# Kernel optimization log

Measured on AMD Instinct MI355X. Metric: run time of the kernel, lower is better.

The kernel has to match this reference:

```python
import jax, jax.numpy as jnp
import numpy as np

N_ENT = 2000
GAT_EMB = 64
GAT_HID = 3
HIDDEN = 256
BATCH = 8
ALPHA = 0.2  # LeakyReLU negative slope
MASK_FILL = jnp.float32(9e-15)  # original fills masked-out logits with 9e-15 (NOT -inf)


def setup_inputs() -> dict:
    key = jax.random.key(0)
    k1, k2, k3, k4, k5, k6 = jax.random.split(key, 6)
    emb = jax.random.normal(k1, (N_ENT, GAT_EMB), dtype=jnp.float32)
    W = jax.random.normal(k2, (GAT_EMB, GAT_HID), dtype=jnp.float32) * 0.2
    a = jax.random.normal(k3, (2 * GAT_HID, 1), dtype=jnp.float32) * 0.2
    fc1_w = jax.random.normal(k4, (HIDDEN, N_ENT * GAT_HID), dtype=jnp.float32) * 0.02
    fc1_b = jax.random.normal(k5, (HIDDEN,), dtype=jnp.float32) * 0.02
    adj = jax.random.randint(k6, (BATCH, N_ENT, N_ENT), 0, 2, dtype=jnp.int32)
    return {"emb": emb, "W": W, "a": a, "fc1_w": fc1_w, "fc1_b": fc1_b, "adj": adj}


def reference(emb, W, a, fc1_w, fc1_b, adj):
    # h = emb @ W : [N, 3] -- shared across all graphs in the batch
    h = emb @ W
    # Pairwise logits: original concatenates [h_i, h_j] and dots with a;
    # equivalent to (h @ a1)_i + (h @ a2)_j via broadcasting (no O(N^2*2H) tensor).
    s1 = h @ a[:GAT_HID, 0]   # [N]
    s2 = h @ a[GAT_HID:, 0]   # [N]
    e = jax.nn.leaky_relu(s1[:, None] + s2[None, :], negative_slope=ALPHA)  # [N, N]
    # Mask by adjacency (fill 9e-15, matching original), softmax over neighbors (dim=1)
    masked = jnp.where(adj > 0, e[None, :, :], MASK_FILL)  # [B, N, N]
    att = jax.nn.softmax(masked, axis=2)
    # Weighted aggregation + ELU (concat=True head)
    h_prime = jnp.einsum('bij,jd->bid', att, h)  # [B, N, 3]
    x = jax.nn.elu(h_prime).reshape(att.shape[0], -1)  # [B, N*3]
    return x @ fc1_w.T + fc1_b  # [B, hidden]
```

## Files before the change

### kernel.cpp

```cpp
#include <hip/hip_runtime.h>
#include <cstddef>

#define N_ENT   2000
#define GAT_EMB 64
#define HIDDEN  256
#define BATCH   8
#define ALPHA   0.2f

typedef _Float16 half4 __attribute__((ext_vector_type(4)));

#define WS_HX_OFF      8192
#define WS_HY_OFF      12288
#define WS_HZ_OFF      16384
#define WS_S1_OFF      20480
#define WS_X_OFF       28672
#define WS_TABLE_BYTES 28672
#define WS_TIER2_BYTES 124672

__global__ __launch_bounds__(256) void k_init(const float* __restrict__ fc1_b,
                                              float* __restrict__ out) {
    int idx = blockIdx.x * 256 + threadIdx.x;
    out[idx] = fc1_b[idx & (HIDDEN - 1)];
}

__global__ __launch_bounds__(256) void k_prep(const float* __restrict__ emb,
                                              const float* __restrict__ W,
                                              const float* __restrict__ a,
                                              float* __restrict__ ws) {
    __shared__ float sW[GAT_EMB * 3];
    __shared__ float sa[6];
    int t = threadIdx.x;
    if (t < GAT_EMB * 3) sW[t] = W[t];
    if (t < 6)           sa[t] = a[t];
    __syncthreads();
    int i = blockIdx.x * 256 + t;
    if (i >= 2048) return;
    if (i >= N_ENT) {
        ws[i] = 0.f;
        ((_Float16*)((char*)ws + WS_HX_OFF))[i] = (_Float16)0;
        ((_Float16*)((char*)ws + WS_HY_OFF))[i] = (_Float16)0;
        ((_Float16*)((char*)ws + WS_HZ_OFF))[i] = (_Float16)0;
        ws[WS_S1_OFF / 4 + i] = 0.f;
        return;
    }
    const float4* er = (const float4*)(emb + (size_t)i * GAT_EMB);
    float h0 = 0.f, h1 = 0.f, h2 = 0.f;
#pragma unroll
    for (int k4 = 0; k4 < GAT_EMB / 4; ++k4) {
        float4 e4 = er[k4];
        int k = 4 * k4;
        h0 += e4.x * sW[(k + 0) * 3 + 0]; h1 += e4.x * sW[(k + 0) * 3 + 1]; h2 += e4.x * sW[(k + 0) * 3 + 2];
        h0 += e4.y * sW[(k + 1) * 3 + 0]; h1 += e4.y * sW[(k + 1) * 3 + 1]; h2 += e4.y * sW[(k + 1) * 3 + 2];
        h0 += e4.z * sW[(k + 2) * 3 + 0]; h1 += e4.z * sW[(k + 2) * 3 + 1]; h2 += e4.z * sW[(k + 2) * 3 + 2];
        h0 += e4.w * sW[(k + 3) * 3 + 0]; h1 += e4.w * sW[(k + 3) * 3 + 1]; h2 += e4.w * sW[(k + 3) * 3 + 2];
    }
    ws[i] = h0 * sa[3] + h1 * sa[4] + h2 * sa[5];
    ((_Float16*)((char*)ws + WS_HX_OFF))[i] = (_Float16)h0;
    ((_Float16*)((char*)ws + WS_HY_OFF))[i] = (_Float16)h1;
    ((_Float16*)((char*)ws + WS_HZ_OFF))[i] = (_Float16)h2;
    ws[WS_S1_OFF / 4 + i] = h0 * sa[0] + h1 * sa[1] + h2 * sa[2];
}

__global__ __launch_bounds__(256, 4) void k_main(const float* __restrict__ emb,
                                                 const float* __restrict__ W,
                                                 const float* __restrict__ a,
                                                 const float* __restrict__ fc1_w,
                                                 const int*   __restrict__ adj,
                                                 float* __restrict__ wsf,
                                                 int mode,
                                                 float* __restrict__ out) {
    __shared__ __align__(16) unsigned char smem[20480];
    float*    s2s = (float*)smem;
    _Float16* hxs = (_Float16*)(smem + 8192);
    _Float16* hys = (_Float16*)(smem + 12288);
    _Float16* hzs = (_Float16*)(smem + 16384);
    __shared__ float sW[GAT_EMB * 3];
    __shared__ float sa[6];
    __shared__ float s1sh[16];
    __shared__ float xblk[48];

    int t = threadIdx.x;
    int R0 = blockIdx.x * 16;
    int b  = R0 / N_ENT;
    int i_base = R0 - b * N_ENT;

    if (mode != 0) {
        const uint4* src = (const uint4*)wsf;
        uint4* dst = (uint4*)smem;
#pragma unroll
        for (int rep = 0; rep < 5; ++rep) dst[rep * 256 + t] = src[rep * 256 + t];
        if (t < 16) s1sh[t] = wsf[WS_S1_OFF / 4 + i_base + t];
    } else {
        if (t < GAT_EMB * 3) sW[t] = W[t];
        if (t < 6)           sa[t] = a[t];
        __syncthreads();
        for (int j = t; j < N_ENT; j += 256) {
            const float4* er = (const float4*)(emb + (size_t)j * GAT_EMB);
            float h0 = 0.f, h1 = 0.f, h2 = 0.f;
#pragma unroll
            for (int k4 = 0; k4 < GAT_EMB / 4; ++k4) {
                float4 e4 = er[k4];
                int k = 4 * k4;
                h0 += e4.x * sW[(k + 0) * 3 + 0]; h1 += e4.x * sW[(k + 0) * 3 + 1]; h2 += e4.x * sW[(k + 0) * 3 + 2];
                h0 += e4.y * sW[(k + 1) * 3 + 0]; h1 += e4.y * sW[(k + 1) * 3 + 1]; h2 += e4.y * sW[(k + 1) * 3 + 2];
                h0 += e4.z * sW[(k + 2) * 3 + 0]; h1 += e4.z * sW[(k + 2) * 3 + 1]; h2 += e4.z * sW[(k + 2) * 3 + 2];
                h0 += e4.w * sW[(k + 3) * 3 + 0]; h1 += e4.w * sW[(k + 3) * 3 + 1]; h2 += e4.w * sW[(k + 3) * 3 + 2];
            }
            s2s[j] = h0 * sa[3] + h1 * sa[4] + h2 * sa[5];
            hxs[j] = (_Float16)h0; hys[j] = (_Float16)h1; hzs[j] = (_Float16)h2;
            if (j >= i_base && j < i_base + 16)
                s1sh[j - i_base] = h0 * sa[0] + h1 * sa[1] + h2 * sa[2];
        }
        if (t < 2048 - N_ENT) {
            int j = N_ENT + t;
            s2s[j] = 0.f; hxs[j] = (_Float16)0; hys[j] = (_Float16)0; hzs[j] = (_Float16)0;
        }
    }
    __syncthreads();

    int lane = t & 63;
    int w    = t >> 6;
    float s1r[4];
    const int* __restrict__ rowp[4];
#pragma unroll
    for (int r = 0; r < 4; ++r) {
        s1r[r] = s1sh[4 * w + r];
        rowp[r] = adj + ((size_t)b * N_ENT + (i_base + 4 * w + r)) * N_ENT;
    }

    float acc[4][4];
#pragma unroll
    for (int r = 0; r < 4; ++r) { acc[r][0] = 0.f; acc[r][1] = 0.f; acc[r][2] = 0.f; acc[r][3] = 0.f; }

    int l4 = lane << 2;
    int4 buf[3][4];
#pragma unroll
    for (int r = 0; r < 4; ++r) buf[0][r] = *(const int4*)(rowp[r] + l4);
#pragma unroll
    for (int r = 0; r < 4; ++r) buf[1][r] = *(const int4*)(rowp[r] + 256 + l4);

#pragma unroll
    for (int c = 0; c < 8; ++c) {
        if (c + 2 < 8) {
            int j2 = (c + 2) * 256 + l4;
            int jc2 = (j2 < N_ENT) ? j2 : 0;
#pragma unroll
            for (int r = 0; r < 4; ++r)
                buf[(c + 2) % 3][r] = *(const int4*)(rowp[r] + jc2);
        }
        int j0 = c * 256 + l4;
        bool valid = (j0 < N_ENT);
        float vw = valid ? 1.0f : 0.0f;
        float4 s2v = *(const float4*)&s2s[j0];
        half4  hxv = *(const half4*)&hxs[j0];
        half4  hyv = *(const half4*)&hys[j0];
        half4  hzv = *(const half4*)&hzs[j0];
        float hx[4], hy[4], hz[4];
#pragma unroll
        for (int q = 0; q < 4; ++q) { hx[q] = (float)hxv[q]; hy[q] = (float)hyv[q]; hz[q] = (float)hzv[q]; }
#pragma unroll
        for (int r = 0; r < 4; ++r) {
            const int* mi = (const int*)&buf[c % 3][r];
#pragma unroll
            for (int q = 0; q < 4; ++q) {
                float e  = s1r[r] + ((const float*)&s2v)[q];
                float ev = __expf(fmaxf(e, 0.f) + ALPHA * fminf(e, 0.f));
                float contrib = ((mi[q] > 0) ? ev : 1.0f) * vw;
                acc[r][0] += contrib;
                acc[r][1] += contrib * hx[q];
                acc[r][2] += contrib * hy[q];
                acc[r][3] += contrib * hz[q];
            }
        }
    }

#pragma unroll
    for (int off = 32; off > 0; off >>= 1)
#pragma unroll
        for (int r = 0; r < 4; ++r) {
            acc[r][0] += __shfl_xor(acc[r][0], off, 64);
            acc[r][1] += __shfl_xor(acc[r][1], off, 64);
            acc[r][2] += __shfl_xor(acc[r][2], off, 64);
            acc[r][3] += __shfl_xor(acc[r][3], off, 64);
        }

    if (lane == 0) {
#pragma unroll
        for (int r = 0; r < 4; ++r) {
            float inv = 1.f / acc[r][0];
            float p0 = acc[r][1] * inv, p1 = acc[r][2] * inv, p2 = acc[r][3] * inv;
            p0 = (p0 > 0.f) ? p0 : expm1f(p0);
            p1 = (p1 > 0.f) ? p1 : expm1f(p1);
            p2 = (p2 > 0.f) ? p2 : expm1f(p2);
            if (mode == 2) {
                _Float16* x16 = (_Float16*)((char*)wsf + WS_X_OFF);
                int i = i_base + 4 * w + r;
                x16[(size_t)(3 * i + 0) * 8 + b] = (_Float16)p0;
                x16[(size_t)(3 * i + 1) * 8 + b] = (_Float16)p1;
                x16[(size_t)(3 * i + 2) * 8 + b] = (_Float16)p2;
            } else {
                int cc = 3 * (4 * w + r);
                xblk[cc + 0] = p0; xblk[cc + 1] = p1; xblk[cc + 2] = p2;
            }
        }
    }

    if (mode != 2) {
        __syncthreads();
        int k = (t + R0) & 255;
        const float* wr = fc1_w + (size_t)k * (N_ENT * 3) + 3 * i_base;
        float d = 0.f;
#pragma unroll
        for (int c4 = 0; c4 < 12; ++c4) {
            float4 wv = *(const float4*)(wr + 4 * c4);
            d += xblk[4 * c4 + 0] * wv.x + xblk[4 * c4 + 1] * wv.y
               + xblk[4 * c4 + 2] * wv.z + xblk[4 * c4 + 3] * wv.w;
        }
        atomicAdd(&out[b * HIDDEN + k], d);
    }
}

__global__ __launch_bounds__(256) void k_fc(const _Float16* __restrict__ x16,
                                            const float* __restrict__ fc1_w,
                                            const float* __restrict__ fc1_b,
                                            float* __restrict__ out) {
    __shared__ float red[4][8];
    int t = threadIdx.x, lane = t & 63, w = t >> 6;
    int k = blockIdx.x;
    const float* __restrict__ wr = fc1_w + (size_t)k * (N_ENT * 3);
    float acc[BATCH];
#pragma unroll
    for (int b = 0; b < BATCH; ++b) acc[b] = 0.f;
#pragma unroll
    for (int it = 0; it < 6; ++it) {
        int m0 = 4 * t + 1024 * it;
        if (m0 + 3 < N_ENT * 3) {
            float4 wv4 = *(const float4*)(wr + m0);
#pragma unroll
            for (int q = 0; q < 4; ++q) {
                half4 xa = *(const half4*)(x16 + (size_t)(m0 + q) * 8);
                half4 xb = *(const half4*)(x16 + (size_t)(m0 + q) * 8 + 4);
                float wv = ((const float*)&wv4)[q];
                acc[0] += wv * (float)xa[0]; acc[1] += wv * (float)xa[1];
                acc[2] += wv * (float)xa[2]; acc[3] += wv * (float)xa[3];
                acc[4] += wv * (float)xb[0]; acc[5] += wv * (float)xb[1];
                acc[6] += wv * (float)xb[2]; acc[7] += wv * (float)xb[3];
            }
        }
    }
#pragma unroll
    for (int off = 32; off > 0; off >>= 1)
#pragma unroll
        for (int b = 0; b < BATCH; ++b) acc[b] += __shfl_xor(acc[b], off, 64);
    if (lane == 0)
#pragma unroll
        for (int b = 0; b < BATCH; ++b) red[w][b] = acc[b];
    __syncthreads();
    if (t < 8)
        out[t * HIDDEN + k] = red[0][t] + red[1][t] + red[2][t] + red[3][t] + fc1_b[k];
}

extern "C" void kernel_launch(void* const* d_in, const int* in_sizes, int n_in,
                              void* d_out, int out_size, void* d_ws, size_t ws_size,
                              hipStream_t stream) {
    const float* emb   = (const float*)d_in[0];
    const float* W     = (const float*)d_in[1];
    const float* a     = (const float*)d_in[2];
    const float* fc1_w = (const float*)d_in[3];
    const float* fc1_b = (const float*)d_in[4];
    const int*   adj   = (const int*)d_in[5];
    float* out = (float*)d_out;
    float* ws  = (float*)d_ws;
    (void)in_sizes; (void)n_in; (void)out_size;

    int tier = (ws_size >= (size_t)WS_TIER2_BYTES) ? 2
             : (ws_size >= (size_t)WS_TABLE_BYTES) ? 1 : 0;

    if (tier < 2)  k_init<<<8, 256, 0, stream>>>(fc1_b, out);
    if (tier >= 1) k_prep<<<8, 256, 0, stream>>>(emb, W, a, ws);
    k_main<<<1000, 256, 0, stream>>>(emb, W, a, fc1_w, adj, ws, tier, out);
    if (tier == 2)
        k_fc<<<HIDDEN, 256, 0, stream>>>((const _Float16*)((char*)d_ws + WS_X_OFF),
                                         fc1_w, fc1_b, out);
}
```

Baseline: 213.2 us.

## Pack adjacency into bitmasks in a separate pass before the GAT kernel

Adds a streaming kernel that reads the int32 adjacency matrix and uses wave ballots to write one bit per edge into a workspace bitmask buffer. The attention kernel then reads these compact masks instead of the full int32 rows, which separates the bandwidth-bound adjacency scan from the exp/accumulate compute. The fused atomic FC path is moved into a fallback kernel that drops the register prefetch ring. This costs one extra launch plus a 4 MB mask write and read, and needs a much larger workspace to run at all.

```diff
diff --git a/kernel.cpp b/kernel.cpp
--- a/kernel.cpp
+++ b/kernel.cpp
@@ -6,16 +6,18 @@
 #define HIDDEN  256
 #define BATCH   8
 #define ALPHA   0.2f
+#define NROWS   (BATCH * N_ENT)
 
 typedef _Float16 half4 __attribute__((ext_vector_type(4)));
+typedef unsigned long long u64;
 
 #define WS_HX_OFF      8192
 #define WS_HY_OFF      12288
 #define WS_HZ_OFF      16384
 #define WS_S1_OFF      20480
 #define WS_X_OFF       28672
-#define WS_TABLE_BYTES 28672
-#define WS_TIER2_BYTES 124672
+#define WS_MASK_OFF    124672
+#define WS_TIER2_BYTES 4220672
 
 __global__ __launch_bounds__(256) void k_init(const float* __restrict__ fc1_b,
                                               float* __restrict__ out) {
@@ -61,14 +63,175 @@
     ws[WS_S1_OFF / 4 + i] = h0 * sa[0] + h1 * sa[1] + h2 * sa[2];
 }
 
-__global__ __launch_bounds__(256, 4) void k_main(const float* __restrict__ emb,
-                                                 const float* __restrict__ W,
-                                                 const float* __restrict__ a,
-                                                 const float* __restrict__ fc1_w,
-                                                 const int*   __restrict__ adj,
-                                                 float* __restrict__ wsf,
-                                                 int mode,
-                                                 float* __restrict__ out) {
+__global__ __launch_bounds__(256) void k_pack(const int* __restrict__ adj,
+                                              u64* __restrict__ masks) {
+    int t = threadIdx.x, lane = t & 63, w = t >> 6;
+    int row = blockIdx.x * 4 + w;
+    const int* __restrict__ rp = adj + (size_t)row * N_ENT;
+    u64* __restrict__ mp = masks + (size_t)row * 32;
+#pragma unroll
+    for (int c = 0; c < 8; ++c) {
+        int j0 = c * 256 + lane * 4;
+        int jc = (j0 < N_ENT) ? j0 : 0;
+        int4 m = *(const int4*)(rp + jc);
+        u64 b0 = __ballot(m.x > 0);
+        u64 b1 = __ballot(m.y > 0);
+        u64 b2 = __ballot(m.z > 0);
+        u64 b3 = __ballot(m.w > 0);
+        if (lane < 4) {
+            u64 v = (lane == 0) ? b0 : (lane == 1) ? b1 : (lane == 2) ? b2 : b3;
+            mp[c * 4 + lane] = v;
+        }
+    }
+}
+
+__global__ __launch_bounds__(256, 4) void k_gat(const u64* __restrict__ masks,
+                                                const float* __restrict__ wsf,
+                                                float* __restrict__ wsx) {
+    __shared__ __align__(16) unsigned char smem[20480];
+    float*    s2s = (float*)smem;
+    _Float16* hxs = (_Float16*)(smem + 8192);
+    _Float16* hys = (_Float16*)(smem + 12288);
+    _Float16* hzs = (_Float16*)(smem + 16384);
+    __shared__ float s1sh[16];
+
+    int t = threadIdx.x;
+    int R0 = blockIdx.x * 16;
+    int b  = R0 / N_ENT;
+    int i_base = R0 - b * N_ENT;
+
+    {
+        const uint4* src = (const uint4*)wsf;
+        uint4* dst = (uint4*)smem;
+#pragma unroll
+        for (int rep = 0; rep < 5; ++rep) dst[rep * 256 + t] = src[rep * 256 + t];
+        if (t < 16) s1sh[t] = wsf[WS_S1_OFF / 4 + i_base + t];
+    }
+    __syncthreads();
+
+    int lane = t & 63;
+    int w    = t >> 6;
+    float s1r[4];
+    const u64* __restrict__ mrow[4];
+#pragma unroll
+    for (int r = 0; r < 4; ++r) {
+        s1r[r] = s1sh[4 * w + r];
+        mrow[r] = masks + (size_t)(R0 + 4 * w + r) * 32;
+    }
+
+    float acc[4][4];
+#pragma unroll
+    for (int r = 0; r < 4; ++r) { acc[r][0] = 0.f; acc[r][1] = 0.f; acc[r][2] = 0.f; acc[r][3] = 0.f; }
+
+    int l4 = lane << 2;
+#pragma unroll
+    for (int c = 0; c < 8; ++c) {
+        int j0 = c * 256 + l4;
+        bool valid = (j0 < N_ENT);
+        float vw = valid ? 1.0f : 0.0f;
+        u64 mq[4][4];
+#pragma unroll
+        for (int r = 0; r < 4; ++r) {
+            ulonglong2 ma = *(const ulonglong2*)(mrow[r] + c * 4);
+            ulonglong2 mb = *(const ulonglong2*)(mrow[r] + c * 4 + 2);
+            mq[r][0] = ma.x; mq[r][1] = ma.y; mq[r][2] = mb.x; mq[r][3] = mb.y;
+        }
+        float4 s2v = *(const float4*)&s2s[j0];
+        half4  hxv = *(const half4*)&hxs[j0];
+        half4  hyv = *(const half4*)&hys[j0];
+        half4  hzv = *(const half4*)&hzs[j0];
+        float hx[4], hy[4], hz[4];
+#pragma unroll
+        for (int q = 0; q < 4; ++q) { hx[q] = (float)hxv[q]; hy[q] = (float)hyv[q]; hz[q] = (float)hzv[q]; }
+#pragma unroll
+        for (int r = 0; r < 4; ++r) {
+#pragma unroll
+            for (int q = 0; q < 4; ++q) {
+                float e  = s1r[r] + ((const float*)&s2v)[q];
+                float ev = __expf(fmaxf(e, 0.f) + ALPHA * fminf(e, 0.f));
+                bool on = (mq[r][q] >> lane) & 1ull;
+                float contrib = (on ? ev : 1.0f) * vw;
+                acc[r][0] += contrib;
+                acc[r][1] += contrib * hx[q];
+                acc[r][2] += contrib * hy[q];
+                acc[r][3] += contrib * hz[q];
+            }
+        }
+    }
+
+#pragma unroll
+    for (int off = 32; off > 0; off >>= 1)
+#pragma unroll
+        for (int r = 0; r < 4; ++r) {
+            acc[r][0] += __shfl_xor(acc[r][0], off, 64);
+            acc[r][1] += __shfl_xor(acc[r][1], off, 64);
+            acc[r][2] += __shfl_xor(acc[r][2], off, 64);
+            acc[r][3] += __shfl_xor(acc[r][3], off, 64);
+        }
+
+    if (lane == 0) {
+        _Float16* x16 = (_Float16*)((char*)wsx + WS_X_OFF);
+#pragma unroll
+        for (int r = 0; r < 4; ++r) {
+            float inv = 1.f / acc[r][0];
+            float p0 = acc[r][1] * inv, p1 = acc[r][2] * inv, p2 = acc[r][3] * inv;
+            p0 = (p0 > 0.f) ? p0 : expm1f(p0);
+            p1 = (p1 > 0.f) ? p1 : expm1f(p1);
+            p2 = (p2 > 0.f) ? p2 : expm1f(p2);
+            int i = i_base + 4 * w + r;
+            x16[(size_t)(3 * i + 0) * 8 + b] = (_Float16)p0;
+            x16[(size_t)(3 * i + 1) * 8 + b] = (_Float16)p1;
+            x16[(size_t)(3 * i + 2) * 8 + b] = (_Float16)p2;
+        }
+    }
+}
+
+__global__ __launch_bounds__(256) void k_fc(const _Float16* __restrict__ x16,
+                                            const float* __restrict__ fc1_w,
+                                            const float* __restrict__ fc1_b,
+                                            float* __restrict__ out) {
+    __shared__ float red[4][8];
+    int t = threadIdx.x, lane = t & 63, w = t >> 6;
+    int k = blockIdx.x;
+    const float* __restrict__ wr = fc1_w + (size_t)k * (N_ENT * 3);
+    float acc[BATCH];
+#pragma unroll
+    for (int b = 0; b < BATCH; ++b) acc[b] = 0.f;
+#pragma unroll
+    for (int it = 0; it < 6; ++it) {
+        int m0 = 4 * t + 1024 * it;
+        if (m0 + 3 < N_ENT * 3) {
+            float4 wv4 = *(const float4*)(wr + m0);
+#pragma unroll
+            for (int q = 0; q < 4; ++q) {
+                half4 xa = *(const half4*)(x16 + (size_t)(m0 + q) * 8);
+                half4 xb = *(const half4*)(x16 + (size_t)(m0 + q) * 8 + 4);
+                float wv = ((const float*)&wv4)[q];
+                acc[0] += wv * (float)xa[0]; acc[1] += wv * (float)xa[1];
+                acc[2] += wv * (float)xa[2]; acc[3] += wv * (float)xa[3];
+                acc[4] += wv * (float)xb[0]; acc[5] += wv * (float)xb[1];
+                acc[6] += wv * (float)xb[2]; acc[7] += wv * (float)xb[3];
+            }
+        }
+    }
+#pragma unroll
+    for (int off = 32; off > 0; off >>= 1)
+#pragma unroll
+        for (int b = 0; b < BATCH; ++b) acc[b] += __shfl_xor(acc[b], off, 64);
+    if (lane == 0)
+#pragma unroll
+        for (int b = 0; b < BATCH; ++b) red[w][b] = acc[b];
+    __syncthreads();
+    if (t < 8)
+        out[t * HIDDEN + k] = red[0][t] + red[1][t] + red[2][t] + red[3][t] + fc1_b[k];
+}
+
+__global__ __launch_bounds__(256, 5) void k_main_fb(const float* __restrict__ emb,
+                                                    const float* __restrict__ W,
+                                                    const float* __restrict__ a,
+                                                    const float* __restrict__ fc1_w,
+                                                    const int*   __restrict__ adj,
+                                                    float* __restrict__ out) {
     __shared__ __align__(16) unsigned char smem[20480];
     float*    s2s = (float*)smem;
     _Float16* hxs = (_Float16*)(smem + 8192);
@@ -84,37 +247,29 @@
     int b  = R0 / N_ENT;
     int i_base = R0 - b * N_ENT;
 
-    if (mode != 0) {
-        const uint4* src = (const uint4*)wsf;
-        uint4* dst = (uint4*)smem;
-#pragma unroll
-        for (int rep = 0; rep < 5; ++rep) dst[rep * 256 + t] = src[rep * 256 + t];
-        if (t < 16) s1sh[t] = wsf[WS_S1_OFF / 4 + i_base + t];
-    } else {
-        if (t < GAT_EMB * 3) sW[t] = W[t];
-        if (t < 6)           sa[t] = a[t];
-        __syncthreads();
-        for (int j = t; j < N_ENT; j += 256) {
-            const float4* er = (const float4*)(emb + (size_t)j * GAT_EMB);
-            float h0 = 0.f, h1 = 0.f, h2 = 0.f;
-#pragma unroll
-            for (int k4 = 0; k4 < GAT_EMB / 4; ++k4) {
-                float4 e4 = er[k4];
-                int k = 4 * k4;
-                h0 += e4.x * sW[(k + 0) * 3 + 0]; h1 += e4.x * sW[(k + 0) * 3 + 1]; h2 += e4.x * sW[(k + 0) * 3 + 2];
-                h0 += e4.y * sW[(k + 1) * 3 + 0]; h1 += e4.y * sW[(k + 1) * 3 + 1]; h2 += e4.y * sW[(k + 1) * 3 + 2];
-                h0 += e4.z * sW[(k + 2) * 3 + 0]; h1 += e4.z * sW[(k + 2) * 3 + 1]; h2 += e4.z * sW[(k + 2) * 3 + 2];
-                h0 += e4.w * sW[(k + 3) * 3 + 0]; h1 += e4.w * sW[(k + 3) * 3 + 1]; h2 += e4.w * sW[(k + 3) * 3 + 2];
-            }
-            s2s[j] = h0 * sa[3] + h1 * sa[4] + h2 * sa[5];
-            hxs[j] = (_Float16)h0; hys[j] = (_Float16)h1; hzs[j] = (_Float16)h2;
-            if (j >= i_base && j < i_base + 16)
-                s1sh[j - i_base] = h0 * sa[0] + h1 * sa[1] + h2 * sa[2];
-        }
-        if (t < 2048 - N_ENT) {
-            int j = N_ENT + t;
-            s2s[j] = 0.f; hxs[j] = (_Float16)0; hys[j] = (_Float16)0; hzs[j] = (_Float16)0;
-        }
+    if (t < GAT_EMB * 3) sW[t] = W[t];
+    if (t < 6)           sa[t] = a[t];
+    __syncthreads();
+    for (int j = t; j < N_ENT; j += 256) {
+        const float4* er = (const float4*)(emb + (size_t)j * GAT_EMB);
+        float h0 = 0.f, h1 = 0.f, h2 = 0.f;
+#pragma unroll
+        for (int k4 = 0; k4 < GAT_EMB / 4; ++k4) {
+            float4 e4 = er[k4];
+            int k = 4 * k4;
+            h0 += e4.x * sW[(k + 0) * 3 + 0]; h1 += e4.x * sW[(k + 0) * 3 + 1]; h2 += e4.x * sW[(k + 0) * 3 + 2];
+            h0 += e4.y * sW[(k + 1) * 3 + 0]; h1 += e4.y * sW[(k + 1) * 3 + 1]; h2 += e4.y * sW[(k + 1) * 3 + 2];
+            h0 += e4.z * sW[(k + 2) * 3 + 0]; h1 += e4.z * sW[(k + 2) * 3 + 1]; h2 += e4.z * sW[(k + 2) * 3 + 2];
+            h0 += e4.w * sW[(k + 3) * 3 + 0]; h1 += e4.w * sW[(k + 3) * 3 + 1]; h2 += e4.w * sW[(k + 3) * 3 + 2];
+        }
+        s2s[j] = h0 * sa[3] + h1 * sa[4] + h2 * sa[5];
+        hxs[j] = (_Float16)h0; hys[j] = (_Float16)h1; hzs[j] = (_Float16)h2;
+        if (j >= i_base && j < i_base + 16)
+            s1sh[j - i_base] = h0 * sa[0] + h1 * sa[1] + h2 * sa[2];
+    }
+    if (t < 2048 - N_ENT) {
+        int j = N_ENT + t;
+        s2s[j] = 0.f; hxs[j] = (_Float16)0; hys[j] = (_Float16)0; hzs[j] = (_Float16)0;
     }
     __syncthreads();
 
@@ -127,30 +282,19 @@
         s1r[r] = s1sh[4 * w + r];
         rowp[r] = adj + ((size_t)b * N_ENT + (i_base + 4 * w + r)) * N_ENT;
     }
-
     float acc[4][4];
 #pragma unroll
     for (int r = 0; r < 4; ++r) { acc[r][0] = 0.f; acc[r][1] = 0.f; acc[r][2] = 0.f; acc[r][3] = 0.f; }
-
     int l4 = lane << 2;
-    int4 buf[3][4];
-#pragma unroll
-    for (int r = 0; r < 4; ++r) buf[0][r] = *(const int4*)(rowp[r] + l4);
-#pragma unroll
-    for (int r = 0; r < 4; ++r) buf[1][r] = *(const int4*)(rowp[r] + 256 + l4);
-
 #pragma unroll
     for (int c = 0; c < 8; ++c) {
-        if (c + 2 < 8) {
-            int j2 = (c + 2) * 256 + l4;
-            int jc2 = (j2 < N_ENT) ? j2 : 0;
-#pragma unroll
-            for (int r = 0; r < 4; ++r)
-                buf[(c + 2) % 3][r] = *(const int4*)(rowp[r] + jc2);
-        }
         int j0 = c * 256 + l4;
         bool valid = (j0 < N_ENT);
-        float vw = valid ? 1.0f : 0.0f;
+        int jc = valid ? j0 : 0;
+        int4 m0 = *(const int4*)(rowp[0] + jc);
+        int4 m1 = *(const int4*)(rowp[1] + jc);
+        int4 m2 = *(const int4*)(rowp[2] + jc);
+        int4 m3 = *(const int4*)(rowp[3] + jc);
         float4 s2v = *(const float4*)&s2s[j0];
         half4  hxv = *(const half4*)&hxs[j0];
         half4  hyv = *(const half4*)&hys[j0];
@@ -158,22 +302,19 @@
         float hx[4], hy[4], hz[4];
 #pragma unroll
         for (int q = 0; q < 4; ++q) { hx[q] = (float)hxv[q]; hy[q] = (float)hyv[q]; hz[q] = (float)hzv[q]; }
-#pragma unroll
-        for (int r = 0; r < 4; ++r) {
-            const int* mi = (const int*)&buf[c % 3][r];
+        const int* mm[4] = { (const int*)&m0, (const int*)&m1, (const int*)&m2, (const int*)&m3 };
+        float vw = valid ? 1.0f : 0.0f;
+#pragma unroll
+        for (int r = 0; r < 4; ++r)
 #pragma unroll
             for (int q = 0; q < 4; ++q) {
                 float e  = s1r[r] + ((const float*)&s2v)[q];
                 float ev = __expf(fmaxf(e, 0.f) + ALPHA * fminf(e, 0.f));
-                float contrib = ((mi[q] > 0) ? ev : 1.0f) * vw;
-                acc[r][0] += contrib;
-                acc[r][1] += contrib * hx[q];
-                acc[r][2] += contrib * hy[q];
-                acc[r][3] += contrib * hz[q];
+                float contrib = ((mm[r][q] > 0) ? ev : 1.0f) * vw;
+                acc[r][0] += contrib; acc[r][1] += contrib * hx[q];
+                acc[r][2] += contrib * hy[q]; acc[r][3] += contrib * hz[q];
             }
-        }
-    }
-
+    }
 #pragma unroll
     for (int off = 32; off > 0; off >>= 1)
 #pragma unroll
@@ -183,81 +324,27 @@
             acc[r][2] += __shfl_xor(acc[r][2], off, 64);
             acc[r][3] += __shfl_xor(acc[r][3], off, 64);
         }
-
-    if (lane == 0) {
+    if (lane == 0)
 #pragma unroll
         for (int r = 0; r < 4; ++r) {
             float inv = 1.f / acc[r][0];
             float p0 = acc[r][1] * inv, p1 = acc[r][2] * inv, p2 = acc[r][3] * inv;
-            p0 = (p0 > 0.f) ? p0 : expm1f(p0);
-            p1 = (p1 > 0.f) ? p1 : expm1f(p1);
-            p2 = (p2 > 0.f) ? p2 : expm1f(p2);
-            if (mode == 2) {
-                _Float16* x16 = (_Float16*)((char*)wsf + WS_X_OFF);
-                int i = i_base + 4 * w + r;
-                x16[(size_t)(3 * i + 0) * 8 + b] = (_Float16)p0;
-                x16[(size_t)(3 * i + 1) * 8 + b] = (_Float16)p1;
-                x16[(size_t)(3 * i + 2) * 8 + b] = (_Float16)p2;
-            } else {
-                int cc = 3 * (4 * w + r);
-                xblk[cc + 0] = p0; xblk[cc + 1] = p1; xblk[cc + 2] = p2;
-            }
-        }
-    }
-
-    if (mode != 2) {
-        __syncthreads();
-        int k = (t + R0) & 255;
-        const float* wr = fc1_w + (size_t)k * (N_ENT * 3) + 3 * i_base;
-        float d = 0.f;
-#pragma unroll
-        for (int c4 = 0; c4 < 12; ++c4) {
-            float4 wv = *(const float4*)(wr + 4 * c4);
-            d += xblk[4 * c4 + 0] * wv.x + xblk[4 * c4 + 1] * wv.y
-               + xblk[4 * c4 + 2] * wv.z + xblk[4 * c4 + 3] * wv.w;
-        }
-        atomicAdd(&out[b * HIDDEN + k], d);
-    }
-}
-
-__global__ __launch_bounds__(256) void k_fc(const _Float16* __restrict__ x16,
-                                            const float* __restrict__ fc1_w,
-                                            const float* __restrict__ fc1_b,
-                                            float* __restrict__ out) {
-    __shared__ float red[4][8];
-    int t = threadIdx.x, lane = t & 63, w = t >> 6;
-    int k = blockIdx.x;
-    const float* __restrict__ wr = fc1_w + (size_t)k * (N_ENT * 3);
-    float acc[BATCH];
-#pragma unroll
-    for (int b = 0; b < BATCH; ++b) acc[b] = 0.f;
-#pragma unroll
-    for (int it = 0; it < 6; ++it) {
-        int m0 = 4 * t + 1024 * it;
-        if (m0 + 3 < N_ENT * 3) {
-            float4 wv4 = *(const float4*)(wr + m0);
-#pragma unroll
-            for (int q = 0; q < 4; ++q) {
-                half4 xa = *(const half4*)(x16 + (size_t)(m0 + q) * 8);
-                half4 xb = *(const half4*)(x16 + (size_t)(m0 + q) * 8 + 4);
-                float wv = ((const float*)&wv4)[q];
-                acc[0] += wv * (float)xa[0]; acc[1] += wv * (float)xa[1];
-                acc[2] += wv * (float)xa[2]; acc[3] += wv * (float)xa[3];
-                acc[4] += wv * (float)xb[0]; acc[5] += wv * (float)xb[1];
-                acc[6] += wv * (float)xb[2]; acc[7] += wv * (float)xb[3];
-            }
-        }
-    }
-#pragma unroll
-    for (int off = 32; off > 0; off >>= 1)
-#pragma unroll
-        for (int b = 0; b < BATCH; ++b) acc[b] += __shfl_xor(acc[b], off, 64);
-    if (lane == 0)
-#pragma unroll
-        for (int b = 0; b < BATCH; ++b) red[w][b] = acc[b];
-    __syncthreads();
-    if (t < 8)
-        out[t * HIDDEN + k] = red[0][t] + red[1][t] + red[2][t] + red[3][t] + fc1_b[k];
+            int cc = 3 * (4 * w + r);
+            xblk[cc + 0] = (p0 > 0.f) ? p0 : expm1f(p0);
+            xblk[cc + 1] = (p1 > 0.f) ? p1 : expm1f(p1);
+            xblk[cc + 2] = (p2 > 0.f) ? p2 : expm1f(p2);
+        }
+    __syncthreads();
+    int k = (t + R0) & 255;
+    const float* wr = fc1_w + (size_t)k * (N_ENT * 3) + 3 * i_base;
+    float d = 0.f;
+#pragma unroll
+    for (int c4 = 0; c4 < 12; ++c4) {
+        float4 wv = *(const float4*)(wr + 4 * c4);
+        d += xblk[4 * c4 + 0] * wv.x + xblk[4 * c4 + 1] * wv.y
+           + xblk[4 * c4 + 2] * wv.z + xblk[4 * c4 + 3] * wv.w;
+    }
+    atomicAdd(&out[b * HIDDEN + k], d);
 }
 
 extern "C" void kernel_launch(void* const* d_in, const int* in_sizes, int n_in,
@@ -273,13 +360,14 @@
     float* ws  = (float*)d_ws;
     (void)in_sizes; (void)n_in; (void)out_size;
 
-    int tier = (ws_size >= (size_t)WS_TIER2_BYTES) ? 2
-             : (ws_size >= (size_t)WS_TABLE_BYTES) ? 1 : 0;
-
-    if (tier < 2)  k_init<<<8, 256, 0, stream>>>(fc1_b, out);
-    if (tier >= 1) k_prep<<<8, 256, 0, stream>>>(emb, W, a, ws);
-    k_main<<<1000, 256, 0, stream>>>(emb, W, a, fc1_w, adj, ws, tier, out);
-    if (tier == 2)
+    if (ws_size >= (size_t)WS_TIER2_BYTES) {
+        k_prep<<<8, 256, 0, stream>>>(emb, W, a, ws);
+        k_pack<<<NROWS / 4, 256, 0, stream>>>(adj, (u64*)((char*)d_ws + WS_MASK_OFF));
+        k_gat<<<1000, 256, 0, stream>>>((const u64*)((char*)d_ws + WS_MASK_OFF), ws, ws);
         k_fc<<<HIDDEN, 256, 0, stream>>>((const _Float16*)((char*)d_ws + WS_X_OFF),
                                          fc1_w, fc1_b, out);
-}
+    } else {
+        k_init<<<8, 256, 0, stream>>>(fc1_b, out);
+        k_main_fb<<<1000, 256, 0, stream>>>(emb, W, a, fc1_w, adj, out);
+    }
+}
```

After: 231.2 us. +8.5%, slower.
